# Kernel tuning notes

Hardware: AMD Instinct MI355X
Metric: run time of the kernel (lower is better)

Reference implementation:

```python
import jax, jax.numpy as jnp
import numpy as np

D = 256          # node_embedding_dim (= GRU hidden per direction)
N = 1024         # number of frame nodes
C = 5            # num_classes
COUNTS = [15, 40, 15]   # num_intervals_per_scale
BINS = [80, 60, 80]     # dist_bins_list
MAX_T = 512      # fixed pad length for per-interval sequences (jit-static)


def _quant(w):
    # int8 per-tensor symmetric fake-quant with straight-through estimator
    s = jnp.maximum(jnp.max(jnp.abs(w)) / 127.0, 1e-8)
    q = jnp.clip(jnp.round(w / s), -128, 127) * s
    return w + jax.lax.stop_gradient(q - w)


def _gru_dir(x, eff, wih, whh, bih, bhh):
    # x: [I, T, D] packed-at-front sequences, eff: [I] valid lengths (>=1)
    # masked scan == torch packed GRU final hidden state
    I, T, _ = x.shape
    H = whh.shape[1]
    valid = jnp.arange(T)[None, :] < eff[:, None]   # [I, T]

    def step(h, inp):
        x_t, v = inp                                # [I,D], [I]
        gi = x_t @ wih.T + bih                      # [I, 3H]
        gh = h @ whh.T + bhh
        ir, iz, inn = jnp.split(gi, 3, axis=1)
        hr, hz, hn = jnp.split(gh, 3, axis=1)
        r = jax.nn.sigmoid(ir + hr)
        z = jax.nn.sigmoid(iz + hz)
        n = jnp.tanh(inn + r * hn)
        h = jnp.where(v[:, None], (1.0 - z) * n + z * h, h)
        return h, None

    h0 = jnp.zeros((I, H), x.dtype)
    hF, _ = jax.lax.scan(step, h0, (jnp.swapaxes(x, 0, 1), valid.T))
    return hF


def _forward(node_embeddings, time_positions, node_pred, audio_len, anchor_intervals,
             gru_wih, gru_whh, gru_bih, gru_bhh, w1, w2,
             w3_s0, w3_s1, w3_s2, sw_s0, ew_s0, sw_s1, ew_s1, sw_s2, ew_s2):
    al = audio_len[0]
    tpos = time_positions[:, 0] * al                     # [N]
    abn = jax.nn.softmax(node_pred, axis=-1)[:, 0]       # abnormal scores [N]
    w3s = [w3_s0, w3_s1, w3_s2]
    sws = [sw_s0, sw_s1, sw_s2]
    ews = [ew_s0, ew_s1, ew_s2]
    offs = np.concatenate([[0], np.cumsum(COUNTS)])
    bounds, confs, clss = [], [], []
    for si in range(3):
        I, b = COUNTS[si], BINS[si]
        anc = anchor_intervals[offs[si]:offs[si + 1]]    # [I, 2]
        starts, ends = anc[:, 0], anc[:, 1]
        # interval membership mask [I, N]
        mask = (tpos[None, :] >= starts[:, None]) & (tpos[None, :] <= ends[:, None])
        # compact valid nodes to the front (stable, preserves node order like x[mask])
        order = jnp.argsort(jnp.logical_not(mask), axis=1, stable=True)[:, :MAX_T]
        msort = jnp.take_along_axis(mask, order, axis=1)
        x_loc = node_embeddings[order] * msort[..., None]   # [I, MAX_T, D]; empty -> zeros row
        eff = jnp.clip(mask.sum(axis=1), 1, MAX_T)          # empty interval behaves as one zero step
        hf = _gru_dir(x_loc, eff, gru_wih[si, 0], gru_whh[si, 0], gru_bih[si, 0], gru_bhh[si, 0])
        # backward direction: reverse each valid prefix
        rev_idx = jnp.clip(eff[:, None] - 1 - jnp.arange(MAX_T)[None, :], 0, MAX_T - 1)
        x_rev = jnp.take_along_axis(x_loc, rev_idx[..., None], axis=1)
        hb = _gru_dir(x_rev, eff, gru_wih[si, 1], gru_whh[si, 1], gru_bih[si, 1], gru_bhh[si, 1])
        # shared feature: [2D | abnormal | center | width | 4 zero pads] = 2D+7
        feat = jnp.concatenate([
            hf, hb,
            abn[:I, None],
            ((starts + ends) * 0.5 / al)[:, None],
            ((ends - starts) / al)[:, None],
            jnp.zeros((I, 4), hf.dtype),
        ], axis=1)
        h = jax.nn.relu(feat @ _quant(w1[si]).T)   # dropout = identity (eval)
        h = jax.nn.relu(h @ _quant(w2[si]).T)
        out = h @ _quant(w3s[si]).T                # [I, 2b+1+(C-1)]
        so = jnp.sum(jax.nn.softmax(out[:, :b], axis=1) * sws[si], axis=1)
        eo = jnp.sum(jax.nn.softmax(out[:, b:2 * b], axis=1) * ews[si], axis=1)
        bounds.append(jnp.stack([jnp.clip(starts + so, 0.0, al), jnp.clip(ends + eo, 0.0, al)], axis=1))
        confs.append(out[:, 2 * b])
        clss.append(out[:, 2 * b + 1:])
    return (jnp.concatenate(bounds, axis=0),   # final_bounds [70, 2]
            jnp.concatenate(confs, axis=0),    # interval_conf_logits [70]
            jnp.concatenate(clss, axis=0))     # interval_cls_logits [70, 4]


def setup_inputs() -> dict:
    key = jax.random.key(0)
    ks = jax.random.split(key, 16)
    inp = {}
    inp["node_embeddings"] = jax.random.normal(ks[0], (N, D), jnp.float32)
    inp["time_positions"] = jax.random.uniform(ks[1], (N, 1), dtype=jnp.float32)
    inp["node_pred"] = jax.random.normal(ks[2], (N, C), jnp.float32)
    inp["audio_len"] = jnp.ones((1,), jnp.float32)
    rng = np.random.default_rng(0)
    widths = [0.05, 0.12, 0.30]
    rows = []
    for c, w in zip(COUNTS, widths):
        s = rng.uniform(0.0, 1.0 - w, size=c).astype(np.float32)
        e = s + rng.uniform(0.5 * w, w, size=c).astype(np.float32)
        rows.append(np.stack([s, e], axis=1))
    inp["anchor_intervals"] = jnp.asarray(np.concatenate(rows, axis=0))
    H = D
    def u(k, shape, fan):
        lim = 1.0 / np.sqrt(fan)
        return jax.random.uniform(k, shape, jnp.float32, -lim, lim)
    # GRU params stacked over [scale, direction]
    inp["gru_wih"] = u(ks[3], (3, 2, 3 * H, D), H)
    inp["gru_whh"] = u(ks[4], (3, 2, 3 * H, H), H)
    inp["gru_bih"] = u(ks[5], (3, 2, 3 * H), H)
    inp["gru_bhh"] = u(ks[6], (3, 2, 3 * H), H)
    F_in = 2 * D + 7
    inp["w1"] = u(ks[7], (3, 256, F_in), F_in)
    inp["w2"] = u(ks[8], (3, 256, 256), 256)
    inp["w3_s0"] = u(ks[9], (2 * BINS[0] + 1 + (C - 1), 256), 256)
    inp["w3_s1"] = u(ks[10], (2 * BINS[1] + 1 + (C - 1), 256), 256)
    inp["w3_s2"] = u(ks[11], (2 * BINS[2] + 1 + (C - 1), 256), 256)
    for i, nb in enumerate(BINS):
        inp[f"sw_s{i}"] = jnp.linspace(-20.0, 20.0, nb, dtype=jnp.float32)
        inp[f"ew_s{i}"] = jnp.linspace(-20.0, 20.0, nb, dtype=jnp.float32)
    return inp


def reference(node_embeddings, time_positions, node_pred, audio_len, anchor_intervals,
              gru_wih, gru_whh, gru_bih, gru_bhh, w1, w2,
              w3_s0, w3_s1, w3_s2, sw_s0, ew_s0, sw_s1, ew_s1, sw_s2, ew_s2):
    return _forward(node_embeddings, time_positions, node_pred, audio_len, anchor_intervals,
                    gru_wih, gru_whh, gru_bih, gru_bhh, w1, w2,
                    w3_s0, w3_s1, w3_s2, sw_s0, ew_s0, sw_s1, ew_s1, sw_s2, ew_s2)
```

## Files before the change

### kernel.cpp

```cpp
#include <hip/hip_runtime.h>
#include <math.h>

#define NN 1024
#define NNP 1025
#define DD 256
#define CC 5
#define G3 768
#define MAXT 512
#define NA 70

typedef _Float16 v8h __attribute__((ext_vector_type(8)));
typedef _Float16 v4h __attribute__((ext_vector_type(4)));
typedef float v4f __attribute__((ext_vector_type(4)));
typedef int v4i __attribute__((ext_vector_type(4)));

__device__ __forceinline__ float sigf(float x){ return __fdividef(1.f, 1.f + __expf(-x)); }
__device__ __forceinline__ float tanhf_fast(float x){ return 1.f - __fdividef(2.f, __expf(2.f*x) + 1.f); }

__global__ __launch_bounds__(256) void mega_kernel(
    const float* __restrict__ node_pred, const float* __restrict__ tp_in,
    const float* __restrict__ audio_len, const float* __restrict__ anchors,
    const float* __restrict__ whh, const float* __restrict__ wih,
    const float* __restrict__ emb,
    const float* __restrict__ bih, const float* __restrict__ bhh,
    const float* __restrict__ w1, const float* __restrict__ w2,
    const float* __restrict__ w30, const float* __restrict__ w31, const float* __restrict__ w32,
    float* __restrict__ abn, int* __restrict__ order, int* __restrict__ cnteff,
    float* __restrict__ qs, float* __restrict__ cm,
    uint4* __restrict__ whhB8, _Float16* __restrict__ E){
  __shared__ __align__(16) unsigned char smem[16*264*2];
  int b = blockIdx.x, tid = threadIdx.x;
  if (b < 4){
    int i = b*256 + tid;
    float pv[CC]; float m = -1e30f;
    for (int c=0;c<CC;++c){ pv[c]=node_pred[i*CC+c]; m=fmaxf(m,pv[c]); }
    float s=0.f;
    for (int c=0;c<CC;++c) s += expf(pv[c]-m);
    abn[i] = expf(pv[0]-m)/s;
  } else if (b < 74){
    if (tid >= 64) return;
    int a = b-4; int lane = tid;
    float al = audio_len[0];
    float s = anchors[2*a], e = anchors[2*a+1];
    int* ord = order + a*MAXT;
    int cnt = 0;
    for (int base=0; base<NN; base+=64){
      float tp = tp_in[base+lane]*al;
      bool msk = (tp>=s)&&(tp<=e);
      unsigned long long bal = __ballot(msk);
      int off = (int)__popcll(bal & ((1ull<<lane)-1ull));
      if (msk && (cnt+off)<MAXT) ord[cnt+off] = base+lane;
      cnt += (int)__popcll(bal);
    }
    if (lane==0){ int c = cnt<MAXT?cnt:MAXT; cnteff[2*a]=c; cnteff[2*a+1]=(c>0)?c:1; }
  } else if (b < 83){
    int m = b-74;
    const float* p; int n;
    if (m<3){ p = w1 + (size_t)m*256*519; n = 256*519; }
    else if (m<6){ p = w2 + (size_t)(m-3)*256*256; n = 256*256; }
    else { p = (m==6)?w30:((m==7)?w31:w32); n = ((m==7)?125:165)*256; }
    float mx = 0.f;
    for (int i=tid;i<n;i+=256) mx = fmaxf(mx, fabsf(p[i]));
    float* red = (float*)smem;
    red[tid]=mx; __syncthreads();
    for (int sft=128; sft>0; sft>>=1){ if (tid<sft) red[tid]=fmaxf(red[tid],red[tid+sft]); __syncthreads(); }
    if (tid==0) qs[m] = fmaxf(red[0]/127.f, 1e-8f);
  } else if (b < 101){
    int i = (b-83)*256 + tid;
    if (i >= 4608) return;
    int gt = i % 3; int c = (i/3)&255; int sd = i/768;
    int j = gt*256 + c;
    float v = bih[sd*G3+j] + ((gt<2)? bhh[sd*G3+j] : 0.f);
    E[((size_t)(sd*NNP + NN))*1024 + c*4 + gt] = (_Float16)v;
  } else if (b < 149){
    int bb = b-101;
    int sd = bb>>3, w = bb&7;
    float* cm_lds = (float*)smem;
    int lane = tid & 63, wv = tid >> 6;
    for (int it=0; it<24; ++it){
      int lr = it*4 + wv;
      int gt = lr>>5, c = lr&31;
      int j = gt*256 + w*32 + c;
      float4 v = reinterpret_cast<const float4*>(whh + ((size_t)sd*G3 + j)*DD)[lane];
      float mx = fmaxf(fmaxf(fabsf(v.x),fabsf(v.y)), fmaxf(fabsf(v.z),fabsf(v.w)));
      #pragma unroll
      for (int sh=1; sh<64; sh<<=1) mx = fmaxf(mx, __shfl_xor(mx, sh));
      if (lane==0){
        float cmax = fmaxf(mx, 1e-12f);
        cm_lds[lr] = cmax;
        cm[sd*G3 + j] = cmax;
      }
    }
    __syncthreads();
    #pragma unroll
    for (int ee=0; ee<6; ++ee){
      int il = tid*6 + ee;
      int q    = il & 3;
      int nt   = (il>>2) % 6;
      int lane2= il / 24;
      int gt = nt>>1, half = nt&1;
      int lr = gt*32 + half*16 + (lane2&15);
      int j  = gt*256 + w*32 + half*16 + (lane2&15);
      int kbase = 64*q + 16*(lane2>>4);
      float inv = 127.f/cm_lds[lr];
      const float* src = whh + ((size_t)sd*G3 + j)*DD + kbase;
      unsigned int dw[4];
      #pragma unroll
      for (int d2=0; d2<4; ++d2){
        unsigned int acc = 0;
        #pragma unroll
        for (int e2=0; e2<4; ++e2){
          float qv = rintf(src[4*d2+e2]*inv);
          qv = fminf(fmaxf(qv,-127.f),127.f);
          int iq = (int)qv;
          acc |= ((unsigned int)(iq & 255)) << (8*e2);
        }
        dw[d2] = acc;
      }
      uint4 v; v.x=dw[0]; v.y=dw[1]; v.z=dw[2]; v.w=dw[3];
      whhB8[(size_t)(sd*8 + w)*1536 + il] = v;
    }
  } else {
    typedef _Float16 AsT[264];
    AsT* As = (AsT*)smem;
    int b2 = b - 149;
    int sd = b2 / 768;
    int rem = b2 - sd*768;
    int r_t = rem & 63, cg = rem >> 6;
    int row0 = r_t*16;
    int lane = tid & 63, wv = tid >> 6;
    int l15 = lane & 15, g16 = lane >> 4;
    {
      int rr = tid>>4, k0 = (tid&15)*16;
      const float4* ep = reinterpret_cast<const float4*>(emb + (size_t)(row0+rr)*DD + k0);
      #pragma unroll
      for (int f=0; f<4; ++f){
        float4 v = ep[f];
        v4h o; o[0]=(_Float16)v.x; o[1]=(_Float16)v.y; o[2]=(_Float16)v.z; o[3]=(_Float16)v.w;
        *reinterpret_cast<v4h*>(&As[rr][k0 + f*4]) = o;
      }
    }
    __syncthreads();
    int c_t = cg*4 + wv;
    int j = c_t*16 + l15;
    const float* Bp = wih + ((size_t)sd*G3 + j)*DD + 8*g16;
    float bsum = bih[sd*G3 + j] + (((j>>8) < 2) ? bhh[sd*G3 + j] : 0.f);
    v4f acc = {0.f,0.f,0.f,0.f};
    #pragma unroll
    for (int q=0;q<8;++q){
      v8h af = *reinterpret_cast<const v8h*>(&As[l15][32*q + 8*g16]);
      float4 b0 = *reinterpret_cast<const float4*>(Bp + 32*q);
      float4 b1 = *reinterpret_cast<const float4*>(Bp + 32*q + 4);
      v8h bf;
      bf[0]=(_Float16)b0.x; bf[1]=(_Float16)b0.y; bf[2]=(_Float16)b0.z; bf[3]=(_Float16)b0.w;
      bf[4]=(_Float16)b1.x; bf[5]=(_Float16)b1.y; bf[6]=(_Float16)b1.z; bf[7]=(_Float16)b1.w;
      acc = __builtin_amdgcn_mfma_f32_16x16x32_f16(af, bf, acc, 0,0,0);
    }
    int gt = j>>8, c = j&255;
    #pragma unroll
    for (int r=0;r<4;++r){
      int row = row0 + g16*4 + r;
      E[((size_t)(sd*NNP + row))*1024 + c*4 + gt] = (_Float16)(acc[r] + bsum);
    }
  }
}

__global__ __launch_bounds__(512, 2) void gru_kernel(
                           const _Float16* __restrict__ E, const v4i* __restrict__ whhB8,
                           const float* __restrict__ bhh, const float* __restrict__ cm,
                           const int* __restrict__ order, const int* __restrict__ cnteff,
                           float* __restrict__ hout){
  int a = blockIdx.x>>1, d = blockIdx.x&1;
  int si = (a<15)?0:((a<55)?1:2);
  int sd = si*2+d;
  int tid = threadIdx.x;
  int w = tid>>6, lane = tid&63;
  int g16 = lane>>4;
  int ct = g16 & 1;

  __shared__ int ord_s[MAXT];
  __shared__ alignas(16) signed char h8[2][DD];

  ord_s[tid] = order[a*MAXT + tid];
  if (tid < DD) h8[0][tid] = 0;

  int cnt = cnteff[2*a], eff = cnteff[2*a+1];

  int c = w*32 + (lane&31);
  float bn = bhh[sd*G3 + 2*DD + c];
  const float ISQ = 1.f/(127.f*127.f);
  float sr = cm[sd*G3 +        c]*ISQ;
  float sz = cm[sd*G3 + 256 +  c]*ISQ;
  float sn = cm[sd*G3 + 512 +  c]*ISQ;

  v4i bf[6][4];
  {
    const v4i* wp = whhB8 + (((size_t)sd*8 + w)*64 + lane)*24;
    #pragma unroll
    for (int nt=0;nt<6;++nt)
      #pragma unroll
      for (int q=0;q<4;++q)
        bf[nt][q] = wp[nt*4+q];
  }

  const uint2* Eb = reinterpret_cast<const uint2*>(E) + (size_t)sd*NNP*256;

  float h = 0.f;
  uint2 gEven, gOdd;
  {
    int idx0 = d ? (eff-1) : 0;
    int n0 = (idx0 < cnt) ? ord_s[idx0] : NN;
    gEven = Eb[(size_t)n0*256 + c];
  }
  __syncthreads();

  for (int t=0;t<eff;++t){
    int p = t & 1;
    if (t+1 < eff){
      int idx1 = d ? (eff-2-t) : (t+1);
      int n1 = (idx1 < cnt) ? ord_s[idx1] : NN;
      if (p==0) gOdd  = Eb[(size_t)n1*256 + c];
      else      gEven = Eb[(size_t)n1*256 + c];
    }
    v4i acc0={0,0,0,0}, acc1={0,0,0,0}, acc2={0,0,0,0};
    v4i acc3={0,0,0,0}, acc4={0,0,0,0}, acc5={0,0,0,0};
    #pragma unroll
    for (int q=0;q<4;++q){
      v4i af = *reinterpret_cast<const v4i*>(&h8[p][64*q + 16*g16]);
      acc0 = __builtin_amdgcn_mfma_i32_16x16x64_i8(af, bf[0][q], acc0, 0,0,0);
      acc1 = __builtin_amdgcn_mfma_i32_16x16x64_i8(af, bf[1][q], acc1, 0,0,0);
      acc2 = __builtin_amdgcn_mfma_i32_16x16x64_i8(af, bf[2][q], acc2, 0,0,0);
      acc3 = __builtin_amdgcn_mfma_i32_16x16x64_i8(af, bf[3][q], acc3, 0,0,0);
      acc4 = __builtin_amdgcn_mfma_i32_16x16x64_i8(af, bf[4][q], acc4, 0,0,0);
      acc5 = __builtin_amdgcn_mfma_i32_16x16x64_i8(af, bf[5][q], acc5, 0,0,0);
    }
    v4h ev = __builtin_bit_cast(v4h, (p==0) ? gEven : gOdd);
    int ir  = (ct==0) ? acc0[0] : acc1[0];
    int iz  = (ct==0) ? acc2[0] : acc3[0];
    int inn = (ct==0) ? acc4[0] : acc5[0];
    float r  = sigf((float)ev[0] + (float)ir*sr);
    float z  = sigf((float)ev[1] + (float)iz*sz);
    float nv = tanhf_fast((float)ev[2] + r*((float)inn*sn + bn));
    h = z*(h - nv) + nv;
    if (lane < 32) h8[p^1][c] = (signed char)(int)rintf(h*127.f);
    __syncthreads();
  }
  if (lane < 32) hout[(size_t)(2*a+d)*DD + c] = h;
}

__global__ __launch_bounds__(512) void mlp_kernel(
    const float* __restrict__ hout, const float* __restrict__ abn,
    const float* __restrict__ anchors, const float* __restrict__ audio_len,
    const float* __restrict__ w1, const float* __restrict__ w2,
    const float* __restrict__ w30, const float* __restrict__ w31, const float* __restrict__ w32,
    const float* __restrict__ qs,
    const float* __restrict__ sw0, const float* __restrict__ ew0,
    const float* __restrict__ sw1, const float* __restrict__ ew1,
    const float* __restrict__ sw2, const float* __restrict__ ew2,
    float* __restrict__ out){
  int bm = blockIdx.x;
  int si = (bm==0)?0:((bm<4)?1:2);
  int mt = (bm==0)?0:((bm<4)?(bm-1):0);
  int cntA = (si==1)?40:15;
  int offA = (si==0)?0:((si==1)?15:55);
  int nout = (si==1)?125:165;
  int bb   = (si==1)?60:80;
  int m0 = mt*16;
  const float* w3 = (si==0)?w30:((si==1)?w31:w32);
  const float* sw = (si==0)?sw0:((si==1)?sw1:sw2);
  const float* ew = (si==0)?ew0:((si==1)?ew1:ew2);
  float al = audio_len[0];

  __shared__ _Float16 feat[16][552];
  __shared__ _Float16 h1s[16][264];
  __shared__ float    os[16][184];

  int tid = threadIdx.x;
  int lane = tid & 63, wv = tid >> 6;
  int l15 = lane & 15, g16 = lane >> 4;

  for (int idx = tid; idx < 16*552; idx += 512){
    int r = idx / 552, c2 = idx - r*552;
    float v = 0.f;
    int m = m0 + r;
    if (m < cntA){
      int a = offA + m;
      if (c2 < 256)       v = hout[(size_t)(2*a)*DD + c2];
      else if (c2 < 512)  v = hout[(size_t)(2*a+1)*DD + (c2-256)];
      else if (c2 == 512) v = abn[m];
      else if (c2 == 513){ float s=anchors[2*a], e=anchors[2*a+1]; v = (s+e)*0.5f/al; }
      else if (c2 == 514){ float s=anchors[2*a], e=anchors[2*a+1]; v = (e-s)/al; }
    }
    feat[r][c2] = (_Float16)v;
  }
  __syncthreads();
  float sc1 = qs[si],   inv1 = 1.f/sc1;
  float sc2 = qs[3+si], inv2 = 1.f/sc2;
  float sc3 = qs[6+si], inv3 = 1.f/sc3;

  for (int nt = wv; nt < 16; nt += 8){
    int j = nt*16 + l15;
    const float* Bp = w1 + ((size_t)(si*256 + j))*519;
    v4f acc = {0.f,0.f,0.f,0.f};
    for (int kq = 0; kq < 17; ++kq){
      int k0 = kq*32 + 8*g16;
      v8h af = *reinterpret_cast<const v8h*>(&feat[l15][k0]);
      v8h bf2;
      #pragma unroll
      for (int e=0;e<8;++e){
        int k = k0 + e;
        float wvv = (k < 519) ? Bp[k] : 0.f;
        float q = rintf(wvv*inv1);
        q = fminf(fmaxf(q,-128.f),127.f);
        bf2[e] = (_Float16)q;
      }
      acc = __builtin_amdgcn_mfma_f32_16x16x32_f16(af, bf2, acc, 0,0,0);
    }
    #pragma unroll
    for (int r=0;r<4;++r) h1s[g16*4+r][j] = (_Float16)fmaxf(acc[r]*sc1, 0.f);
  }
  __syncthreads();
  for (int nt = wv; nt < 16; nt += 8){
    int j = nt*16 + l15;
    const float* Bp = w2 + ((size_t)(si*256 + j))*256;
    v4f acc = {0.f,0.f,0.f,0.f};
    for (int kq = 0; kq < 8; ++kq){
      int k0 = kq*32 + 8*g16;
      v8h af = *reinterpret_cast<const v8h*>(&h1s[l15][k0]);
      v8h bf2;
      #pragma unroll
      for (int e=0;e<8;++e){
        float q = rintf(Bp[k0+e]*inv2);
        q = fminf(fmaxf(q,-128.f),127.f);
        bf2[e] = (_Float16)q;
      }
      acc = __builtin_amdgcn_mfma_f32_16x16x32_f16(af, bf2, acc, 0,0,0);
    }
    #pragma unroll
    for (int r=0;r<4;++r) feat[g16*4+r][j] = (_Float16)fmaxf(acc[r]*sc2, 0.f);
  }
  __syncthreads();
  for (int nt = wv; nt < 11; nt += 8){
    int j = nt*16 + l15;
    bool jv = (j < nout);
    const float* Bp = w3 + (size_t)j*256;
    v4f acc = {0.f,0.f,0.f,0.f};
    for (int kq = 0; kq < 8; ++kq){
      int k0 = kq*32 + 8*g16;
      v8h af = *reinterpret_cast<const v8h*>(&feat[l15][k0]);
      v8h bf2;
      #pragma unroll
      for (int e=0;e<8;++e){
        float wvv = jv ? Bp[k0+e] : 0.f;
        float q = rintf(wvv*inv3);
        q = fminf(fmaxf(q,-128.f),127.f);
        bf2[e] = (_Float16)q;
      }
      acc = __builtin_amdgcn_mfma_f32_16x16x32_f16(af, bf2, acc, 0,0,0);
    }
    #pragma unroll
    for (int r=0;r<4;++r) os[g16*4+r][j] = acc[r]*sc3;
  }
  __syncthreads();
  for (int lm = wv; lm < 16; lm += 8){
    int m = m0 + lm;
    if (m >= cntA) continue;
    int a = offA + m;
    float s = anchors[2*a], e = anchors[2*a+1];
    float x0 = (lane < bb) ? os[lm][lane] : -1e30f;
    float x1 = (lane+64 < bb) ? os[lm][lane+64] : -1e30f;
    float mx = fmaxf(x0, x1);
    #pragma unroll
    for (int sh=1; sh<64; sh<<=1) mx = fmaxf(mx, __shfl_xor(mx, sh));
    float e0 = (lane < bb) ? expf(x0-mx) : 0.f;
    float e1 = (lane+64 < bb) ? expf(x1-mx) : 0.f;
    float se = e0 + e1;
    float ws2 = e0*((lane<bb)?sw[lane]:0.f) + e1*((lane+64<bb)?sw[lane+64]:0.f);
    #pragma unroll
    for (int sh=1; sh<64; sh<<=1){ se += __shfl_xor(se, sh); ws2 += __shfl_xor(ws2, sh); }
    float so = ws2/se;
    float y0 = (lane < bb) ? os[lm][bb+lane] : -1e30f;
    float y1 = (lane+64 < bb) ? os[lm][bb+lane+64] : -1e30f;
    float my = fmaxf(y0, y1);
    #pragma unroll
    for (int sh=1; sh<64; sh<<=1) my = fmaxf(my, __shfl_xor(my, sh));
    float f0 = (lane < bb) ? expf(y0-my) : 0.f;
    float f1 = (lane+64 < bb) ? expf(y1-my) : 0.f;
    float sf = f0 + f1;
    float wf = f0*((lane<bb)?ew[lane]:0.f) + f1*((lane+64<bb)?ew[lane+64]:0.f);
    #pragma unroll
    for (int sh=1; sh<64; sh<<=1){ sf += __shfl_xor(sf, sh); wf += __shfl_xor(wf, sh); }
    float eo = wf/sf;
    if (lane == 0){
      out[2*a]   = fminf(fmaxf(s+so, 0.f), al);
      out[2*a+1] = fminf(fmaxf(e+eo, 0.f), al);
      out[140+a] = os[lm][2*bb];
    }
    if (lane < 4) out[210+4*a+lane] = os[lm][2*bb+1+lane];
  }
}

extern "C" void kernel_launch(void* const* d_in, const int* in_sizes, int n_in,
                              void* d_out, int out_size, void* d_ws, size_t ws_size,
                              hipStream_t stream){
  const float* emb   = (const float*)d_in[0];
  const float* tpin  = (const float*)d_in[1];
  const float* npred = (const float*)d_in[2];
  const float* alen  = (const float*)d_in[3];
  const float* anch  = (const float*)d_in[4];
  const float* wih   = (const float*)d_in[5];
  const float* whh   = (const float*)d_in[6];
  const float* bih   = (const float*)d_in[7];
  const float* bhh   = (const float*)d_in[8];
  const float* w1    = (const float*)d_in[9];
  const float* w2    = (const float*)d_in[10];
  const float* w30   = (const float*)d_in[11];
  const float* w31   = (const float*)d_in[12];
  const float* w32   = (const float*)d_in[13];
  const float* sw0   = (const float*)d_in[14];
  const float* ew0   = (const float*)d_in[15];
  const float* sw1   = (const float*)d_in[16];
  const float* ew1   = (const float*)d_in[17];
  const float* sw2   = (const float*)d_in[18];
  const float* ew2   = (const float*)d_in[19];

  char* ws = (char*)d_ws;
  size_t off = 0;
  auto take = [&](size_t bytes)->char*{
    char* p = ws + off;
    off = (off + bytes + 255) & ~(size_t)255;
    return p;
  };
  float* abn    = (float*)take((size_t)NN*4);
  int*   order_ = (int*)  take((size_t)NA*MAXT*4);
  int*   cnteff = (int*)  take((size_t)NA*2*4);
  float* qs     = (float*)take(16*4);
  float* cm     = (float*)take((size_t)6*G3*4);
  uint4* whhB8  = (uint4*)take((size_t)6*8*64*24*16);
  _Float16* E   = (_Float16*)take((size_t)6*NNP*1024*2);
  float* hout   = (float*)take((size_t)NA*2*DD*4);
  (void)ws_size; (void)in_sizes; (void)n_in; (void)out_size;

  mega_kernel<<<dim3(4757), dim3(256), 0, stream>>>(npred, tpin, alen, anch, whh, wih, emb,
                                                    bih, bhh, w1, w2, w30, w31, w32,
                                                    abn, order_, cnteff, qs, cm, whhB8, E);
  gru_kernel<<<dim3(NA*2), dim3(512), 0, stream>>>(E, (const v4i*)whhB8, bhh, cm, order_, cnteff, hout);
  mlp_kernel<<<dim3(5), dim3(512), 0, stream>>>(hout, abn, anch, alen, w1, w2, w30, w31, w32, qs,
                                                sw0, ew0, sw1, ew1, sw2, ew2, (float*)d_out);
}
```

Baseline: 418.6 us.

## Shrink GRU blocks to 4 waves with 12 MFMA tiles; prepack MLP weights

The GRU recurrence block drops from 8 waves of 512 threads to 4 waves of 256 threads. Each wave now holds twice as many int8 Whh fragments (12 tiles) in registers, and every lane owns one hidden unit instead of half the lanes idling. The Whh packing in the mega kernel is re-laid out to match. Separately, the quantised fp16 MFMA fragments for w1/w2/w3 are precomputed by extra blocks launched alongside the GRU blocks. This lets the MLP kernel load packed fragments directly instead of quantising weights inside its inner loops. The risks are higher register pressure per wave, longer per-wave MFMA chains in the serial recurrence, and extra global traffic for the packed weights.

```diff
diff --git a/kernel.cpp b/kernel.cpp
--- a/kernel.cpp
+++ b/kernel.cpp
@@ -13,6 +13,10 @@
 typedef _Float16 v4h __attribute__((ext_vector_type(4)));
 typedef float v4f __attribute__((ext_vector_type(4)));
 typedef int v4i __attribute__((ext_vector_type(4)));
+
+#define NF1 (3*16*17*64)
+#define NF2 (3*16*8*64)
+#define NF3 (3*11*8*64)
 
 __device__ __forceinline__ float sigf(float x){ return __fdividef(1.f, 1.f + __expf(-x)); }
 __device__ __forceinline__ float tanhf_fast(float x){ return 1.f - __fdividef(2.f, __expf(2.f*x) + 1.f); }
@@ -72,15 +76,15 @@
     int j = gt*256 + c;
     float v = bih[sd*G3+j] + ((gt<2)? bhh[sd*G3+j] : 0.f);
     E[((size_t)(sd*NNP + NN))*1024 + c*4 + gt] = (_Float16)v;
-  } else if (b < 149){
+  } else if (b < 125){
     int bb = b-101;
-    int sd = bb>>3, w = bb&7;
+    int sd = bb>>2, w = bb&3;
     float* cm_lds = (float*)smem;
     int lane = tid & 63, wv = tid >> 6;
-    for (int it=0; it<24; ++it){
+    for (int it=0; it<48; ++it){
       int lr = it*4 + wv;
-      int gt = lr>>5, c = lr&31;
-      int j = gt*256 + w*32 + c;
+      int gt = lr>>6, cc = lr&63;
+      int j = gt*256 + w*64 + cc;
       float4 v = reinterpret_cast<const float4*>(whh + ((size_t)sd*G3 + j)*DD)[lane];
       float mx = fmaxf(fmaxf(fabsf(v.x),fabsf(v.y)), fmaxf(fabsf(v.z),fabsf(v.w)));
       #pragma unroll
@@ -93,14 +97,13 @@
     }
     __syncthreads();
     #pragma unroll
-    for (int ee=0; ee<6; ++ee){
-      int il = tid*6 + ee;
-      int q    = il & 3;
-      int nt   = (il>>2) % 6;
-      int lane2= il / 24;
-      int gt = nt>>1, half = nt&1;
-      int lr = gt*32 + half*16 + (lane2&15);
-      int j  = gt*256 + w*32 + half*16 + (lane2&15);
+    for (int ee=0; ee<12; ++ee){
+      int il = tid*12 + ee;
+      int lane2 = il/48; int rr = il - lane2*48;
+      int nt = rr>>2; int q = rr&3;
+      int gt = nt>>2, s = nt&3;
+      int j  = gt*256 + w*64 + s*16 + (lane2&15);
+      int lr = gt*64  + s*16 + (lane2&15);
       int kbase = 64*q + 16*(lane2>>4);
       float inv = 127.f/cm_lds[lr];
       const float* src = whh + ((size_t)sd*G3 + j)*DD + kbase;
@@ -118,12 +121,12 @@
         dw[d2] = acc;
       }
       uint4 v; v.x=dw[0]; v.y=dw[1]; v.z=dw[2]; v.w=dw[3];
-      whhB8[(size_t)(sd*8 + w)*1536 + il] = v;
+      whhB8[(size_t)(sd*4 + w)*3072 + il] = v;
     }
   } else {
     typedef _Float16 AsT[264];
     AsT* As = (AsT*)smem;
-    int b2 = b - 149;
+    int b2 = b - 125;
     int sd = b2 / 768;
     int rem = b2 - sd*768;
     int r_t = rem & 63, cg = rem >> 6;
@@ -165,45 +168,111 @@
   }
 }
 
-__global__ __launch_bounds__(512, 2) void gru_kernel(
-                           const _Float16* __restrict__ E, const v4i* __restrict__ whhB8,
-                           const float* __restrict__ bhh, const float* __restrict__ cm,
-                           const int* __restrict__ order, const int* __restrict__ cnteff,
-                           float* __restrict__ hout){
-  int a = blockIdx.x>>1, d = blockIdx.x&1;
+__global__ __launch_bounds__(256, 1) void gru_kernel(
+    const _Float16* __restrict__ E, const v4i* __restrict__ whhB8,
+    const float* __restrict__ bhh, const float* __restrict__ cm,
+    const int* __restrict__ order, const int* __restrict__ cnteff,
+    float* __restrict__ hout,
+    const float* __restrict__ w1, const float* __restrict__ w2,
+    const float* __restrict__ w30, const float* __restrict__ w31, const float* __restrict__ w32,
+    const float* __restrict__ qs,
+    v8h* __restrict__ w1F, v8h* __restrict__ w2F, v8h* __restrict__ w3F){
+  int blk = blockIdx.x;
+  int tid = threadIdx.x;
+  if (blk >= NA*2){
+    int i = (blk - NA*2)*256 + tid;
+    if (i < NF1){
+      int lane = i & 63; int rest = i >> 6;
+      int q = rest % 17; int rc = rest / 17;
+      int ct = rc & 15; int si = rc >> 4;
+      int j = ct*16 + (lane&15);
+      int k0 = q*32 + 8*(lane>>4);
+      float inv = 1.f/qs[si];
+      const float* src = w1 + ((size_t)(si*256 + j))*519;
+      v8h o;
+      #pragma unroll
+      for (int e=0;e<8;++e){
+        int k = k0+e;
+        float wv = (k<519)? src[k] : 0.f;
+        float qv = rintf(wv*inv);
+        qv = fminf(fmaxf(qv,-128.f),127.f);
+        o[e] = (_Float16)qv;
+      }
+      w1F[i] = o;
+    } else if (i < NF1+NF2){
+      int r = i - NF1;
+      int lane = r & 63; int rest = r >> 6;
+      int q = rest & 7; int rc = rest >> 3;
+      int ct = rc & 15; int si = rc >> 4;
+      int j = ct*16 + (lane&15);
+      int k0 = q*32 + 8*(lane>>4);
+      float inv = 1.f/qs[3+si];
+      const float* src = w2 + ((size_t)(si*256 + j))*256 + k0;
+      v8h o;
+      #pragma unroll
+      for (int e=0;e<8;++e){
+        float qv = rintf(src[e]*inv);
+        qv = fminf(fmaxf(qv,-128.f),127.f);
+        o[e] = (_Float16)qv;
+      }
+      w2F[r] = o;
+    } else if (i < NF1+NF2+NF3){
+      int r = i - NF1 - NF2;
+      int lane = r & 63; int rest = r >> 6;
+      int q = rest & 7; int rc = rest >> 3;
+      int ct = rc % 11; int si = rc / 11;
+      int j = ct*16 + (lane&15);
+      int nout = (si==1)?125:165;
+      const float* w3 = (si==0)?w30:((si==1)?w31:w32);
+      int k0 = q*32 + 8*(lane>>4);
+      float inv = 1.f/qs[6+si];
+      v8h o;
+      #pragma unroll
+      for (int e=0;e<8;++e){
+        float wv = (j<nout)? w3[(size_t)j*256 + k0+e] : 0.f;
+        float qv = rintf(wv*inv);
+        qv = fminf(fmaxf(qv,-128.f),127.f);
+        o[e] = (_Float16)qv;
+      }
+      w3F[r] = o;
+    }
+    return;
+  }
+  int a = blk>>1, d = blk&1;
   int si = (a<15)?0:((a<55)?1:2);
   int sd = si*2+d;
-  int tid = threadIdx.x;
   int w = tid>>6, lane = tid&63;
-  int g16 = lane>>4;
-  int ct = g16 & 1;
+  int g16 = lane>>4, l15 = lane&15;
 
   __shared__ int ord_s[MAXT];
   __shared__ alignas(16) signed char h8[2][DD];
 
-  ord_s[tid] = order[a*MAXT + tid];
-  if (tid < DD) h8[0][tid] = 0;
+  ord_s[tid]     = order[a*MAXT + tid];
+  ord_s[tid+256] = order[a*MAXT + tid + 256];
+  h8[0][tid] = 0;
 
   int cnt = cnteff[2*a], eff = cnteff[2*a+1];
 
-  int c = w*32 + (lane&31);
+  int c = w*64 + g16*16 + l15;
   float bn = bhh[sd*G3 + 2*DD + c];
   const float ISQ = 1.f/(127.f*127.f);
-  float sr = cm[sd*G3 +        c]*ISQ;
-  float sz = cm[sd*G3 + 256 +  c]*ISQ;
-  float sn = cm[sd*G3 + 512 +  c]*ISQ;
-
-  v4i bf[6][4];
+  float sr = cm[sd*G3 +       c]*ISQ;
+  float sz = cm[sd*G3 + 256 + c]*ISQ;
+  float sn = cm[sd*G3 + 512 + c]*ISQ;
+
+  v4i bf[12][4];
   {
-    const v4i* wp = whhB8 + (((size_t)sd*8 + w)*64 + lane)*24;
-    #pragma unroll
-    for (int nt=0;nt<6;++nt)
+    const v4i* wp = whhB8 + (((size_t)sd*4 + w)*64 + lane)*48;
+    #pragma unroll
+    for (int nt=0;nt<12;++nt)
       #pragma unroll
       for (int q=0;q<4;++q)
         bf[nt][q] = wp[nt*4+q];
   }
 
   const uint2* Eb = reinterpret_cast<const uint2*>(E) + (size_t)sd*NNP*256;
+
+  __syncthreads();
 
   float h = 0.f;
   uint2 gEven, gOdd;
@@ -212,7 +281,6 @@
     int n0 = (idx0 < cnt) ? ord_s[idx0] : NN;
     gEven = Eb[(size_t)n0*256 + c];
   }
-  __syncthreads();
 
   for (int t=0;t<eff;++t){
     int p = t & 1;
@@ -222,37 +290,43 @@
       if (p==0) gOdd  = Eb[(size_t)n1*256 + c];
       else      gEven = Eb[(size_t)n1*256 + c];
     }
-    v4i acc0={0,0,0,0}, acc1={0,0,0,0}, acc2={0,0,0,0};
-    v4i acc3={0,0,0,0}, acc4={0,0,0,0}, acc5={0,0,0,0};
+    v4i a0={0,0,0,0}, a1={0,0,0,0}, a2={0,0,0,0}, a3={0,0,0,0};
+    v4i a4={0,0,0,0}, a5={0,0,0,0}, a6={0,0,0,0}, a7={0,0,0,0};
+    v4i a8={0,0,0,0}, a9={0,0,0,0}, a10={0,0,0,0}, a11={0,0,0,0};
     #pragma unroll
     for (int q=0;q<4;++q){
       v4i af = *reinterpret_cast<const v4i*>(&h8[p][64*q + 16*g16]);
-      acc0 = __builtin_amdgcn_mfma_i32_16x16x64_i8(af, bf[0][q], acc0, 0,0,0);
-      acc1 = __builtin_amdgcn_mfma_i32_16x16x64_i8(af, bf[1][q], acc1, 0,0,0);
-      acc2 = __builtin_amdgcn_mfma_i32_16x16x64_i8(af, bf[2][q], acc2, 0,0,0);
-      acc3 = __builtin_amdgcn_mfma_i32_16x16x64_i8(af, bf[3][q], acc3, 0,0,0);
-      acc4 = __builtin_amdgcn_mfma_i32_16x16x64_i8(af, bf[4][q], acc4, 0,0,0);
-      acc5 = __builtin_amdgcn_mfma_i32_16x16x64_i8(af, bf[5][q], acc5, 0,0,0);
+      a0  = __builtin_amdgcn_mfma_i32_16x16x64_i8(af, bf[0][q],  a0,  0,0,0);
+      a1  = __builtin_amdgcn_mfma_i32_16x16x64_i8(af, bf[1][q],  a1,  0,0,0);
+      a2  = __builtin_amdgcn_mfma_i32_16x16x64_i8(af, bf[2][q],  a2,  0,0,0);
+      a3  = __builtin_amdgcn_mfma_i32_16x16x64_i8(af, bf[3][q],  a3,  0,0,0);
+      a4  = __builtin_amdgcn_mfma_i32_16x16x64_i8(af, bf[4][q],  a4,  0,0,0);
+      a5  = __builtin_amdgcn_mfma_i32_16x16x64_i8(af, bf[5][q],  a5,  0,0,0);
+      a6  = __builtin_amdgcn_mfma_i32_16x16x64_i8(af, bf[6][q],  a6,  0,0,0);
+      a7  = __builtin_amdgcn_mfma_i32_16x16x64_i8(af, bf[7][q],  a7,  0,0,0);
+      a8  = __builtin_amdgcn_mfma_i32_16x16x64_i8(af, bf[8][q],  a8,  0,0,0);
+      a9  = __builtin_amdgcn_mfma_i32_16x16x64_i8(af, bf[9][q],  a9,  0,0,0);
+      a10 = __builtin_amdgcn_mfma_i32_16x16x64_i8(af, bf[10][q], a10, 0,0,0);
+      a11 = __builtin_amdgcn_mfma_i32_16x16x64_i8(af, bf[11][q], a11, 0,0,0);
     }
     v4h ev = __builtin_bit_cast(v4h, (p==0) ? gEven : gOdd);
-    int ir  = (ct==0) ? acc0[0] : acc1[0];
-    int iz  = (ct==0) ? acc2[0] : acc3[0];
-    int inn = (ct==0) ? acc4[0] : acc5[0];
+    int ir  = (g16==0)?a0[0]:((g16==1)?a1[0]:((g16==2)?a2[0]:a3[0]));
+    int iz  = (g16==0)?a4[0]:((g16==1)?a5[0]:((g16==2)?a6[0]:a7[0]));
+    int inn = (g16==0)?a8[0]:((g16==1)?a9[0]:((g16==2)?a10[0]:a11[0]));
     float r  = sigf((float)ev[0] + (float)ir*sr);
     float z  = sigf((float)ev[1] + (float)iz*sz);
     float nv = tanhf_fast((float)ev[2] + r*((float)inn*sn + bn));
     h = z*(h - nv) + nv;
-    if (lane < 32) h8[p^1][c] = (signed char)(int)rintf(h*127.f);
+    h8[p^1][c] = (signed char)(int)rintf(h*127.f);
     __syncthreads();
   }
-  if (lane < 32) hout[(size_t)(2*a+d)*DD + c] = h;
+  hout[(size_t)(2*a+d)*DD + c] = h;
 }
 
 __global__ __launch_bounds__(512) void mlp_kernel(
     const float* __restrict__ hout, const float* __restrict__ abn,
     const float* __restrict__ anchors, const float* __restrict__ audio_len,
-    const float* __restrict__ w1, const float* __restrict__ w2,
-    const float* __restrict__ w30, const float* __restrict__ w31, const float* __restrict__ w32,
+    const v8h* __restrict__ w1F, const v8h* __restrict__ w2F, const v8h* __restrict__ w3F,
     const float* __restrict__ qs,
     const float* __restrict__ sw0, const float* __restrict__ ew0,
     const float* __restrict__ sw1, const float* __restrict__ ew1,
@@ -263,10 +337,8 @@
   int mt = (bm==0)?0:((bm<4)?(bm-1):0);
   int cntA = (si==1)?40:15;
   int offA = (si==0)?0:((si==1)?15:55);
-  int nout = (si==1)?125:165;
   int bb   = (si==1)?60:80;
   int m0 = mt*16;
-  const float* w3 = (si==0)?w30:((si==1)?w31:w32);
   const float* sw = (si==0)?sw0:((si==1)?sw1:sw2);
   const float* ew = (si==0)?ew0:((si==1)?ew1:ew2);
   float al = audio_len[0];
@@ -294,27 +366,15 @@
     feat[r][c2] = (_Float16)v;
   }
   __syncthreads();
-  float sc1 = qs[si],   inv1 = 1.f/sc1;
-  float sc2 = qs[3+si], inv2 = 1.f/sc2;
-  float sc3 = qs[6+si], inv3 = 1.f/sc3;
+  float sc1 = qs[si], sc2 = qs[3+si], sc3 = qs[6+si];
 
   for (int nt = wv; nt < 16; nt += 8){
     int j = nt*16 + l15;
-    const float* Bp = w1 + ((size_t)(si*256 + j))*519;
+    const v8h* bp = w1F + (size_t)(si*16 + nt)*17*64 + lane;
     v4f acc = {0.f,0.f,0.f,0.f};
     for (int kq = 0; kq < 17; ++kq){
-      int k0 = kq*32 + 8*g16;
-      v8h af = *reinterpret_cast<const v8h*>(&feat[l15][k0]);
-      v8h bf2;
-      #pragma unroll
-      for (int e=0;e<8;++e){
-        int k = k0 + e;
-        float wvv = (k < 519) ? Bp[k] : 0.f;
-        float q = rintf(wvv*inv1);
-        q = fminf(fmaxf(q,-128.f),127.f);
-        bf2[e] = (_Float16)q;
-      }
-      acc = __builtin_amdgcn_mfma_f32_16x16x32_f16(af, bf2, acc, 0,0,0);
+      v8h af = *reinterpret_cast<const v8h*>(&feat[l15][kq*32 + 8*g16]);
+      acc = __builtin_amdgcn_mfma_f32_16x16x32_f16(af, bp[kq*64], acc, 0,0,0);
     }
     #pragma unroll
     for (int r=0;r<4;++r) h1s[g16*4+r][j] = (_Float16)fmaxf(acc[r]*sc1, 0.f);
@@ -322,19 +382,11 @@
   __syncthreads();
   for (int nt = wv; nt < 16; nt += 8){
     int j = nt*16 + l15;
-    const float* Bp = w2 + ((size_t)(si*256 + j))*256;
+    const v8h* bp = w2F + (size_t)(si*16 + nt)*8*64 + lane;
     v4f acc = {0.f,0.f,0.f,0.f};
     for (int kq = 0; kq < 8; ++kq){
-      int k0 = kq*32 + 8*g16;
-      v8h af = *reinterpret_cast<const v8h*>(&h1s[l15][k0]);
-      v8h bf2;
-      #pragma unroll
-      for (int e=0;e<8;++e){
-        float q = rintf(Bp[k0+e]*inv2);
-        q = fminf(fmaxf(q,-128.f),127.f);
-        bf2[e] = (_Float16)q;
-      }
-      acc = __builtin_amdgcn_mfma_f32_16x16x32_f16(af, bf2, acc, 0,0,0);
+      v8h af = *reinterpret_cast<const v8h*>(&h1s[l15][kq*32 + 8*g16]);
+      acc = __builtin_amdgcn_mfma_f32_16x16x32_f16(af, bp[kq*64], acc, 0,0,0);
     }
     #pragma unroll
     for (int r=0;r<4;++r) feat[g16*4+r][j] = (_Float16)fmaxf(acc[r]*sc2, 0.f);
@@ -342,21 +394,11 @@
   __syncthreads();
   for (int nt = wv; nt < 11; nt += 8){
     int j = nt*16 + l15;
-    bool jv = (j < nout);
-    const float* Bp = w3 + (size_t)j*256;
+    const v8h* bp = w3F + (size_t)(si*11 + nt)*8*64 + lane;
     v4f acc = {0.f,0.f,0.f,0.f};
     for (int kq = 0; kq < 8; ++kq){
-      int k0 = kq*32 + 8*g16;
-      v8h af = *reinterpret_cast<const v8h*>(&feat[l15][k0]);
-      v8h bf2;
-      #pragma unroll
-      for (int e=0;e<8;++e){
-        float wvv = jv ? Bp[k0+e] : 0.f;
-        float q = rintf(wvv*inv3);
-        q = fminf(fmaxf(q,-128.f),127.f);
-        bf2[e] = (_Float16)q;
-      }
-      acc = __builtin_amdgcn_mfma_f32_16x16x32_f16(af, bf2, acc, 0,0,0);
+      v8h af = *reinterpret_cast<const v8h*>(&feat[l15][kq*32 + 8*g16]);
+      acc = __builtin_amdgcn_mfma_f32_16x16x32_f16(af, bp[kq*64], acc, 0,0,0);
     }
     #pragma unroll
     for (int r=0;r<4;++r) os[g16*4+r][j] = acc[r]*sc3;
@@ -436,15 +478,23 @@
   int*   cnteff = (int*)  take((size_t)NA*2*4);
   float* qs     = (float*)take(16*4);
   float* cm     = (float*)take((size_t)6*G3*4);
-  uint4* whhB8  = (uint4*)take((size_t)6*8*64*24*16);
+  uint4* whhB8  = (uint4*)take((size_t)6*4*3072*16);
   _Float16* E   = (_Float16*)take((size_t)6*NNP*1024*2);
   float* hout   = (float*)take((size_t)NA*2*DD*4);
+  v8h* w1F      = (v8h*)take((size_t)NF1*16);
+  v8h* w2F      = (v8h*)take((size_t)NF2*16);
+  v8h* w3F      = (v8h*)take((size_t)NF3*16);
   (void)ws_size; (void)in_sizes; (void)n_in; (void)out_size;
 
-  mega_kernel<<<dim3(4757), dim3(256), 0, stream>>>(npred, tpin, alen, anch, whh, wih, emb,
+  mega_kernel<<<dim3(4733), dim3(256), 0, stream>>>(npred, tpin, alen, anch, whh, wih, emb,
                                                     bih, bhh, w1, w2, w30, w31, w32,
                                                     abn, order_, cnteff, qs, cm, whhB8, E);
-  gru_kernel<<<dim3(NA*2), dim3(512), 0, stream>>>(E, (const v4i*)whhB8, bhh, cm, order_, cnteff, hout);
-  mlp_kernel<<<dim3(5), dim3(512), 0, stream>>>(hout, abn, anch, alen, w1, w2, w30, w31, w32, qs,
+  {
+    const int packBlocks = (NF1+NF2+NF3+255)/256;
+    gru_kernel<<<dim3(NA*2 + packBlocks), dim3(256), 0, stream>>>(
+        E, (const v4i*)whhB8, bhh, cm, order_, cnteff, hout,
+        w1, w2, w30, w31, w32, qs, w1F, w2F, w3F);
+  }
+  mlp_kernel<<<dim3(5), dim3(512), 0, stream>>>(hout, abn, anch, alen, w1F, w2F, w3F, qs,
                                                 sw0, ew0, sw1, ew1, sw2, ew2, (float*)d_out);
 }
```

Result: faster. 410.1 us (-2.0%).
